# Optimization experiments

Hardware: AMD Instinct MI355X
Metric: run time of the kernel (lower is better)

## Reference

```python
import jax, jax.numpy as jnp
import numpy as np

B, S, D = 4, 2048, 1024
H = 16
DH = D // H

def setup_inputs() -> dict:
    key = jax.random.key(0)
    ks = jax.random.split(key, 5)
    s = 1.0 / np.sqrt(D)
    return {
        "inputs": jax.random.normal(ks[0], (B, S, D), dtype=jnp.float32),
        "Wq": jax.random.normal(ks[1], (D, D), dtype=jnp.float32) * s,
        "Wk": jax.random.normal(ks[2], (D, D), dtype=jnp.float32) * s,
        "Wv": jax.random.normal(ks[3], (D, D), dtype=jnp.float32) * s,
        "Wo": jax.random.normal(ks[4], (D, D), dtype=jnp.float32) * s,
        "bo": jnp.zeros((D,), dtype=jnp.float32),
    }

def reference(inputs, Wq, Wk, Wv, Wo, bo):
    b, s, _ = inputs.shape
    # nn.Linear: y = x @ W.T (no bias for QKV)
    Q = (inputs @ Wq.T).reshape(b, s, H, DH)
    K = (inputs @ Wk.T).reshape(b, s, H, DH)
    V = (inputs @ Wv.T).reshape(b, s, H, DH)
    scores = jnp.einsum("bqhd,bkhd->bhqk", Q, K)  # [B,H,S,S]
    causal = jnp.triu(jnp.ones((s, s), dtype=bool), k=1)
    scores = jnp.where(causal, -jnp.inf, scores)
    w = jax.nn.softmax(scores / np.sqrt(DH), axis=-1)  # dropout p=0.0 -> identity
    Z = jnp.einsum("bhqk,bkhd->bqhd", w, V).reshape(b, s, D)
    return Z @ Wo.T + bo
```

## Files before the change

### kernel.cpp

```cpp
#include <hip/hip_runtime.h>
#include <hip/hip_bf16.h>


#define Bq 4
#define Sq 2048
#define Dq 1024
#define Hq 16
#define DHq 64

typedef __attribute__((ext_vector_type(8))) short short8;
typedef __attribute__((ext_vector_type(4))) float f32x4;
typedef __attribute__((ext_vector_type(4))) unsigned short ushort4v;
typedef __attribute__((ext_vector_type(2))) unsigned int uint2v;

static __device__ __forceinline__ unsigned short f2bfu(float f) {
    union { __hip_bfloat16 h; unsigned short u; } cv;
    cv.h = __float2bfloat16(f);
    return cv.u;
}
static __device__ __forceinline__ unsigned int cvtpk(float lo, float hi) {
    unsigned int r;
    asm("v_cvt_pk_bf16_f32 %0, %1, %2" : "=v"(r) : "v"(lo), "v"(hi));
    return r;
}

__global__ __launch_bounds__(256) void tobf16(
    const float* __restrict__ X, const float* __restrict__ W0,
    const float* __restrict__ W1, const float* __restrict__ W2,
    const float* __restrict__ W3,
    unsigned short* __restrict__ xb, unsigned short* __restrict__ wb)
{
    const size_t i = ((size_t)blockIdx.x * 256 + threadIdx.x) * 8;
    const size_t NX = (size_t)8388608;
    const float* src; unsigned short* dst; size_t off;
    if (i < NX) { src = X; dst = xb; off = i; }
    else {
        const size_t j = i - NX;
        const int w = (int)(j >> 20);
        off = j & 1048575;
        src = (w == 0) ? W0 : (w == 1) ? W1 : (w == 2) ? W2 : W3;
        dst = wb + ((size_t)w << 20);
    }
    const float4 a = *reinterpret_cast<const float4*>(src + off);
    const float4 b = *reinterpret_cast<const float4*>(src + off + 4);
    short8 v;
    v[0] = (short)f2bfu(a.x); v[1] = (short)f2bfu(a.y);
    v[2] = (short)f2bfu(a.z); v[3] = (short)f2bfu(a.w);
    v[4] = (short)f2bfu(b.x); v[5] = (short)f2bfu(b.y);
    v[6] = (short)f2bfu(b.z); v[7] = (short)f2bfu(b.w);
    *reinterpret_cast<short8*>(dst + off) = v;
}



__global__ __launch_bounds__(256) void mm_qkv(
    const unsigned short* __restrict__ Ab, const unsigned short* __restrict__ Wall,
    unsigned short* __restrict__ oq, unsigned short* __restrict__ ok,
    unsigned short* __restrict__ ovt)
{
    __shared__ unsigned short As[128 * 64];
    __shared__ unsigned short Bs[128 * 64];

    const int z = blockIdx.z;
    const unsigned short* W = Wall + ((size_t)z << 20);

    const int m0 = blockIdx.x * 128, n0 = blockIdx.y * 128;
    const int t = threadIdx.x, lane = t & 63, wave = t >> 6;
    const int g = lane >> 4, c = lane & 15;
    const int wm = wave >> 1, wn = wave & 1;
    const int r8 = lane >> 3, c8 = lane & 7;
    const int ss = (c8 ^ (r8 & 7)) * 8;

    f32x4 acc[4][4] = {};

    for (int kt = 0; kt < 16; ++kt) {
        const int kb = kt * 64;
#pragma unroll
        for (int p = 0; p < 4; ++p) {
            const int rowb = wave * 8 + p * 32;
            const unsigned short* ga = Ab + (size_t)(m0 + rowb + r8) * 1024 + kb + ss;
            const unsigned short* gb = W  + (size_t)(n0 + rowb + r8) * 1024 + kb + ss;
            __builtin_amdgcn_global_load_lds(
                (const __attribute__((address_space(1))) unsigned int*)ga,
                (__attribute__((address_space(3))) unsigned int*)(As + rowb * 64), 16, 0, 0);
            __builtin_amdgcn_global_load_lds(
                (const __attribute__((address_space(1))) unsigned int*)gb,
                (__attribute__((address_space(3))) unsigned int*)(Bs + rowb * 64), 16, 0, 0);
        }
        __syncthreads();
        if (z != 2) {
#pragma unroll
            for (int ks = 0; ks < 2; ++ks) {
                const int sa = ((ks * 4 + g) ^ (c & 7)) * 8;
                short8 bf[4];
#pragma unroll
                for (int nt = 0; nt < 4; ++nt)
                    bf[nt] = *reinterpret_cast<const short8*>(&Bs[(wn * 64 + nt * 16 + c) * 64 + sa]);
#pragma unroll
                for (int mt = 0; mt < 4; ++mt) {
                    const short8 af = *reinterpret_cast<const short8*>(&As[(wm * 64 + mt * 16 + c) * 64 + sa]);
#pragma unroll
                    for (int nt = 0; nt < 4; ++nt)
                        acc[mt][nt] = __builtin_amdgcn_mfma_f32_16x16x32_bf16(af, bf[nt], acc[mt][nt], 0, 0, 0);
                }
            }
        } else {
#pragma unroll
            for (int ks = 0; ks < 2; ++ks) {
                const int sa = ((ks * 4 + g) ^ (c & 7)) * 8;
                short8 bf[4];
#pragma unroll
                for (int nt = 0; nt < 4; ++nt)
                    bf[nt] = *reinterpret_cast<const short8*>(&Bs[(wn * 64 + nt * 16 + c) * 64 + sa]);
#pragma unroll
                for (int mt = 0; mt < 4; ++mt) {
                    const short8 af = *reinterpret_cast<const short8*>(&As[(wm * 64 + mt * 16 + c) * 64 + sa]);
#pragma unroll
                    for (int nt = 0; nt < 4; ++nt)
                        acc[mt][nt] = __builtin_amdgcn_mfma_f32_16x16x32_bf16(bf[nt], af, acc[mt][nt], 0, 0, 0);
                }
            }
        }
        __syncthreads();
    }

    if (z == 2) {
#pragma unroll
        for (int mt = 0; mt < 4; ++mt)
#pragma unroll
            for (int nt = 0; nt < 4; ++nt)
#pragma unroll
                for (int r = 0; r < 4; ++r) {
                    const int m = m0 + wm * 64 + mt * 16 + c;
                    const int n = n0 + wn * 64 + nt * 16 + g * 4 + r;
                    const int bb = m >> 11, s = m & 2047;
                    const int h = n >> 6, d = n & 63;
                    const size_t off = (size_t)(bb * Hq + h) * 131072
                        + (s >> 6) * 4096 + ((d >> 4) & 3) * 1024 + ((s >> 5) & 1) * 512
                        + ((s >> 3) & 3) * 128 + (d & 15) * 8 + (s & 7);
                    ovt[off] = f2bfu(acc[mt][nt][r]);
                }
    } else {
        const float oscale = (z == 0) ? 0.180336880f : 1.0f;
        unsigned short* out = z ? ok : oq;
#pragma unroll
        for (int mt = 0; mt < 4; ++mt)
#pragma unroll
            for (int nt = 0; nt < 4; ++nt)
#pragma unroll
                for (int r = 0; r < 4; ++r) {
                    const int m = m0 + wm * 64 + mt * 16 + g * 4 + r;
                    const int n = n0 + wn * 64 + nt * 16 + c;
                    const int bb = m >> 11, s = m & 2047;
                    const int h = n >> 6, d = n & 63;
                    const size_t off = (size_t)(bb * Hq + h) * 131072
                        + (s >> 4) * 1024 + (d >> 5) * 512 + ((d >> 3) & 3) * 128
                        + (s & 15) * 8 + (d & 7);
                    out[off] = f2bfu(acc[mt][nt][r] * oscale);
                }
    }
}

static __device__ __forceinline__ void stage_kv8(
    const unsigned short* __restrict__ Kb, const unsigned short* __restrict__ Vb,
    int kb, unsigned short* kl, unsigned short* vl, int wave, int lane)
{
    const int off = wave * 512 + lane * 8;
    __builtin_amdgcn_global_load_lds(
        (const __attribute__((address_space(1))) unsigned int*)(Kb + (size_t)kb * 4096 + off),
        (__attribute__((address_space(3))) unsigned int*)(kl + wave * 512), 16, 0, 0);
    __builtin_amdgcn_global_load_lds(
        (const __attribute__((address_space(1))) unsigned int*)(Vb + (size_t)kb * 4096 + off),
        (__attribute__((address_space(3))) unsigned int*)(vl + wave * 512), 16, 0, 0);
}

static __device__ __forceinline__ void qtile(
    const short8* kf, const short8* vf, const short8 q0, const short8 q1,
    int rel, int g, int c, unsigned short (*PtW)[72],
    f32x4* oacc, f32x4& lacc, const short8 onesf)
{
    f32x4 st[4] = {};
#pragma unroll
    for (int k2 = 0; k2 < 4; ++k2) {
        st[k2] = __builtin_amdgcn_mfma_f32_16x16x32_bf16(kf[2 * k2],     q0, st[k2], 0, 0, 0);
        st[k2] = __builtin_amdgcn_mfma_f32_16x16x32_bf16(kf[2 * k2 + 1], q1, st[k2], 0, 0, 0);
    }

    if (rel < 4) {
        const int lim = rel * 16 + c;
#pragma unroll
        for (int kt = 0; kt < 4; ++kt)
#pragma unroll
            for (int r = 0; r < 4; ++r)
                if (kt * 16 + g * 4 + r > lim) st[kt][r] = -3.0e38f;
    }

#pragma unroll
    for (int kt = 0; kt < 4; ++kt) {
        uint2v u;
        u[0] = cvtpk(exp2f(st[kt][0]), exp2f(st[kt][1]));
        u[1] = cvtpk(exp2f(st[kt][2]), exp2f(st[kt][3]));
        *reinterpret_cast<uint2v*>(&PtW[c][kt * 16 + g * 4]) = u;
    }
    const short8 pb0 = *reinterpret_cast<const short8*>(&PtW[c][g * 8]);
    const short8 pb1 = *reinterpret_cast<const short8*>(&PtW[c][32 + g * 8]);

#pragma unroll
    for (int dt = 0; dt < 4; ++dt) {
        oacc[dt] = __builtin_amdgcn_mfma_f32_16x16x32_bf16(vf[2 * dt],     pb0, oacc[dt], 0, 0, 0);
        oacc[dt] = __builtin_amdgcn_mfma_f32_16x16x32_bf16(vf[2 * dt + 1], pb1, oacc[dt], 0, 0, 0);
    }
    lacc = __builtin_amdgcn_mfma_f32_16x16x32_bf16(onesf, pb0, lacc, 0, 0, 0);
    lacc = __builtin_amdgcn_mfma_f32_16x16x32_bf16(onesf, pb1, lacc, 0, 0, 0);
}

__global__ __launch_bounds__(512) void attn(
    const unsigned short* __restrict__ Qf, const unsigned short* __restrict__ Kf,
    const unsigned short* __restrict__ Vf, unsigned short* __restrict__ O)
{
    __shared__ unsigned short Kl[2][4096];
    __shared__ unsigned short Vl[2][4096];
    __shared__ unsigned short Pt[8][2][16][72];

    const int bid = blockIdx.x;
    const int pair = (bid >> 3) & 3;
    const int bh = (bid & 7) | ((bid >> 5) << 3);

    const int t = threadIdx.x, lane = t & 63, wave = t >> 6;
    const int g = lane >> 4, c = lane & 15;
    const size_t base = (size_t)bh * (Sq * DHq);
    const unsigned short* Qb = Qf + base;
    const unsigned short* Kb = Kf + base;
    const unsigned short* Vb = Vf + base;
    const int b = bh >> 4, h = bh & 15;

    short8 onesf;
#pragma unroll
    for (int j = 0; j < 8; ++j) onesf[j] = (short)0x3F80;

#pragma unroll 1
    for (int pp = 0; pp < 2; ++pp) {
        const int qi = pp ? (3 - pair) + 4 : pair;
        const int qi2 = pp ? (7 - pair) : pair;
        const int qq = qi2;
        const int qtA = qq * 16 + wave * 2;
        const int qtB = qtA + 1;
        (void)qi;

        const unsigned short* qpA = Qb + (size_t)qtA * 1024 + lane * 8;
        const unsigned short* qpB = Qb + (size_t)qtB * 1024 + lane * 8;
        const short8 qA0 = *reinterpret_cast<const short8*>(qpA);
        const short8 qA1 = *reinterpret_cast<const short8*>(qpA + 512);
        const short8 qB0 = *reinterpret_cast<const short8*>(qpB);
        const short8 qB1 = *reinterpret_cast<const short8*>(qpB + 512);

        f32x4 oA[4] = {}, oB[4] = {};
        f32x4 lA = {}, lB = {};

        const int ibmax = 4 * qq + 3;

        stage_kv8(Kb, Vb, 0, Kl[0], Vl[0], wave, lane);
        __syncthreads();

#pragma unroll 1
        for (int ib = 0; ib <= ibmax; ++ib) {
            const int cur = ib & 1;
            if (ib < ibmax)
                stage_kv8(Kb, Vb, ib + 1, Kl[cur ^ 1], Vl[cur ^ 1], wave, lane);
            __builtin_amdgcn_sched_barrier(0);

            if (4 * ib <= qtB) {
                short8 kf[8], vf[8];
#pragma unroll
                for (int i = 0; i < 8; ++i)
                    kf[i] = *reinterpret_cast<const short8*>(&Kl[cur][lane * 8 + i * 512]);
#pragma unroll
                for (int i = 0; i < 8; ++i)
                    vf[i] = *reinterpret_cast<const short8*>(&Vl[cur][lane * 8 + i * 512]);

                if (4 * ib <= qtA)
                    qtile(kf, vf, qA0, qA1, qtA - 4 * ib, g, c, Pt[wave][0], oA, lA, onesf);
                qtile(kf, vf, qB0, qB1, qtB - 4 * ib, g, c, Pt[wave][1], oB, lB, onesf);
            }
            __syncthreads();
        }

        const float rlA = 1.0f / lA[0];
        const float rlB = 1.0f / lB[0];
        const size_t orowA = ((size_t)b * Sq + qtA * 16 + c) * Dq + h * 64;
        const size_t orowB = ((size_t)b * Sq + qtB * 16 + c) * Dq + h * 64;
#pragma unroll
        for (int dt = 0; dt < 4; ++dt) {
            uint2v uA, uB;
            uA[0] = cvtpk(oA[dt][0] * rlA, oA[dt][1] * rlA);
            uA[1] = cvtpk(oA[dt][2] * rlA, oA[dt][3] * rlA);
            uB[0] = cvtpk(oB[dt][0] * rlB, oB[dt][1] * rlB);
            uB[1] = cvtpk(oB[dt][2] * rlB, oB[dt][3] * rlB);
            *reinterpret_cast<uint2v*>(&O[orowA + dt * 16 + g * 4]) = uA;
            *reinterpret_cast<uint2v*>(&O[orowB + dt * 16 + g * 4]) = uB;
        }
    }
}

__global__ __launch_bounds__(256) void mm_o(
    const unsigned short* __restrict__ Ab, const unsigned short* __restrict__ Wall,
    const float* __restrict__ bo, float* __restrict__ outf)
{
    __shared__ unsigned short As[128 * 64];
    __shared__ unsigned short Bs[128 * 64];

    const unsigned short* W = Wall + ((size_t)3 << 20);

    const int m0 = blockIdx.x * 128, n0 = blockIdx.y * 128;
    const int t = threadIdx.x, lane = t & 63, wave = t >> 6;
    const int g = lane >> 4, c = lane & 15;
    const int wm = wave >> 1, wn = wave & 1;
    const int r8 = lane >> 3, c8 = lane & 7;
    const int ss = (c8 ^ (r8 & 7)) * 8;

    f32x4 acc[4][4] = {};

    for (int kt = 0; kt < 16; ++kt) {
        const int kb = kt * 64;
#pragma unroll
        for (int p = 0; p < 4; ++p) {
            const int rowb = wave * 8 + p * 32;
            const unsigned short* ga = Ab + (size_t)(m0 + rowb + r8) * 1024 + kb + ss;
            const unsigned short* gb = W  + (size_t)(n0 + rowb + r8) * 1024 + kb + ss;
            __builtin_amdgcn_global_load_lds(
                (const __attribute__((address_space(1))) unsigned int*)ga,
                (__attribute__((address_space(3))) unsigned int*)(As + rowb * 64), 16, 0, 0);
            __builtin_amdgcn_global_load_lds(
                (const __attribute__((address_space(1))) unsigned int*)gb,
                (__attribute__((address_space(3))) unsigned int*)(Bs + rowb * 64), 16, 0, 0);
        }
        __syncthreads();
#pragma unroll
        for (int ks = 0; ks < 2; ++ks) {
            const int sa = ((ks * 4 + g) ^ (c & 7)) * 8;
            short8 bf[4];
#pragma unroll
            for (int nt = 0; nt < 4; ++nt)
                bf[nt] = *reinterpret_cast<const short8*>(&Bs[(wn * 64 + nt * 16 + c) * 64 + sa]);
#pragma unroll
            for (int mt = 0; mt < 4; ++mt) {
                const short8 af = *reinterpret_cast<const short8*>(&As[(wm * 64 + mt * 16 + c) * 64 + sa]);
#pragma unroll
                for (int nt = 0; nt < 4; ++nt)
                    acc[mt][nt] = __builtin_amdgcn_mfma_f32_16x16x32_bf16(af, bf[nt], acc[mt][nt], 0, 0, 0);
            }
        }
        __syncthreads();
    }

#pragma unroll
    for (int nt = 0; nt < 4; ++nt) {
        const int n = n0 + wn * 64 + nt * 16 + c;
        const float bias = bo[n];
#pragma unroll
        for (int mt = 0; mt < 4; ++mt)
#pragma unroll
            for (int r = 0; r < 4; ++r) {
                const int m = m0 + wm * 64 + mt * 16 + g * 4 + r;
                outf[(size_t)m * 1024 + n] = acc[mt][nt][r] + bias;
            }
    }
}

extern "C" void kernel_launch(void* const* d_in, const int* in_sizes, int n_in,
                              void* d_out, int out_size, void* d_ws, size_t ws_size,
                              hipStream_t stream) {
    const float* X  = (const float*)d_in[0];
    const float* Wq = (const float*)d_in[1];
    const float* Wk = (const float*)d_in[2];
    const float* Wv = (const float*)d_in[3];
    const float* Wo = (const float*)d_in[4];
    const float* bo = (const float*)d_in[5];
    float* out = (float*)d_out;

    const size_t elems = (size_t)Bq * Hq * Sq * DHq;
    unsigned short* q  = (unsigned short*)d_ws;
    unsigned short* k  = q + elems;
    unsigned short* vt = k + elems;
    unsigned short* xo = vt + elems;
    unsigned short* wb = xo + elems;

    tobf16<<<dim3(6144), 256, 0, stream>>>(X, Wq, Wk, Wv, Wo, xo, wb);

    mm_qkv<<<dim3(64, 8, 3), 256, 0, stream>>>(xo, wb, q, k, vt);

    attn<<<dim3(256), 512, 0, stream>>>(q, k, vt, xo);

    mm_o<<<dim3(64, 8, 1), 256, 0, stream>>>(xo, wb, bo, out);
}
```

Baseline: 187.5 us.

## Split attention blocks to one query chunk each and load V fragments lazily

The attention kernel no longer processes a balanced pair of query chunks per block. It launches 512 blocks with one 256-row query chunk each, ordered heaviest-first. V fragments are now read from LDS inside qtile just before their MFMAs rather than preloaded into registers, and launch bounds request 4 waves per SIMD to raise occupancy. This trades the pairwise causal load balancing for more parallelism and lower register pressure, but blocks now have uneven work and V may be re-read from LDS for each of the two q-tiles.

```diff
diff --git a/kernel.cpp b/kernel.cpp
--- a/kernel.cpp
+++ b/kernel.cpp
@@ -175,8 +175,9 @@
 }
 
 static __device__ __forceinline__ void qtile(
-    const short8* kf, const short8* vf, const short8 q0, const short8 q1,
-    int rel, int g, int c, unsigned short (*PtW)[72],
+    const short8* kf, const unsigned short* __restrict__ vl,
+    const short8 q0, const short8 q1,
+    int rel, int g, int c, int lane, unsigned short (*PtW)[72],
     f32x4* oacc, f32x4& lacc, const short8 onesf)
 {
     f32x4 st[4] = {};
@@ -207,14 +208,16 @@
 
 #pragma unroll
     for (int dt = 0; dt < 4; ++dt) {
-        oacc[dt] = __builtin_amdgcn_mfma_f32_16x16x32_bf16(vf[2 * dt],     pb0, oacc[dt], 0, 0, 0);
-        oacc[dt] = __builtin_amdgcn_mfma_f32_16x16x32_bf16(vf[2 * dt + 1], pb1, oacc[dt], 0, 0, 0);
+        const short8 vf0 = *reinterpret_cast<const short8*>(&vl[lane * 8 + (2 * dt) * 512]);
+        const short8 vf1 = *reinterpret_cast<const short8*>(&vl[lane * 8 + (2 * dt + 1) * 512]);
+        oacc[dt] = __builtin_amdgcn_mfma_f32_16x16x32_bf16(vf0, pb0, oacc[dt], 0, 0, 0);
+        oacc[dt] = __builtin_amdgcn_mfma_f32_16x16x32_bf16(vf1, pb1, oacc[dt], 0, 0, 0);
     }
     lacc = __builtin_amdgcn_mfma_f32_16x16x32_bf16(onesf, pb0, lacc, 0, 0, 0);
     lacc = __builtin_amdgcn_mfma_f32_16x16x32_bf16(onesf, pb1, lacc, 0, 0, 0);
 }
 
-__global__ __launch_bounds__(512) void attn(
+__global__ __launch_bounds__(512, 4) void attn(
     const unsigned short* __restrict__ Qf, const unsigned short* __restrict__ Kf,
     const unsigned short* __restrict__ Vf, unsigned short* __restrict__ O)
 {
@@ -223,8 +226,8 @@
     __shared__ unsigned short Pt[8][2][16][72];
 
     const int bid = blockIdx.x;
-    const int pair = (bid >> 3) & 3;
-    const int bh = (bid & 7) | ((bid >> 5) << 3);
+    const int qq = 7 - ((bid >> 3) & 7);
+    const int bh = (bid & 7) | ((bid >> 6) << 3);
 
     const int t = threadIdx.x, lane = t & 63, wave = t >> 6;
     const int g = lane >> 4, c = lane & 15;
@@ -238,67 +241,57 @@
 #pragma unroll
     for (int j = 0; j < 8; ++j) onesf[j] = (short)0x3F80;
 
+    const int qtA = qq * 16 + wave * 2;
+    const int qtB = qtA + 1;
+
+    const unsigned short* qpA = Qb + (size_t)qtA * 1024 + lane * 8;
+    const unsigned short* qpB = Qb + (size_t)qtB * 1024 + lane * 8;
+    const short8 qA0 = *reinterpret_cast<const short8*>(qpA);
+    const short8 qA1 = *reinterpret_cast<const short8*>(qpA + 512);
+    const short8 qB0 = *reinterpret_cast<const short8*>(qpB);
+    const short8 qB1 = *reinterpret_cast<const short8*>(qpB + 512);
+
+    f32x4 oA[4] = {}, oB[4] = {};
+    f32x4 lA = {}, lB = {};
+
+    const int ibmax = 4 * qq + 3;
+
+    stage_kv8(Kb, Vb, 0, Kl[0], Vl[0], wave, lane);
+    __syncthreads();
+
 #pragma unroll 1
-    for (int pp = 0; pp < 2; ++pp) {
-        const int qi = pp ? (3 - pair) + 4 : pair;
-        const int qi2 = pp ? (7 - pair) : pair;
-        const int qq = qi2;
-        const int qtA = qq * 16 + wave * 2;
-        const int qtB = qtA + 1;
-        (void)qi;
-
-        const unsigned short* qpA = Qb + (size_t)qtA * 1024 + lane * 8;
-        const unsigned short* qpB = Qb + (size_t)qtB * 1024 + lane * 8;
-        const short8 qA0 = *reinterpret_cast<const short8*>(qpA);
-        const short8 qA1 = *reinterpret_cast<const short8*>(qpA + 512);
-        const short8 qB0 = *reinterpret_cast<const short8*>(qpB);
-        const short8 qB1 = *reinterpret_cast<const short8*>(qpB + 512);
-
-        f32x4 oA[4] = {}, oB[4] = {};
-        f32x4 lA = {}, lB = {};
-
-        const int ibmax = 4 * qq + 3;
-
-        stage_kv8(Kb, Vb, 0, Kl[0], Vl[0], wave, lane);
-        __syncthreads();
-
-#pragma unroll 1
-        for (int ib = 0; ib <= ibmax; ++ib) {
-            const int cur = ib & 1;
-            if (ib < ibmax)
-                stage_kv8(Kb, Vb, ib + 1, Kl[cur ^ 1], Vl[cur ^ 1], wave, lane);
-            __builtin_amdgcn_sched_barrier(0);
-
-            if (4 * ib <= qtB) {
-                short8 kf[8], vf[8];
-#pragma unroll
-                for (int i = 0; i < 8; ++i)
-                    kf[i] = *reinterpret_cast<const short8*>(&Kl[cur][lane * 8 + i * 512]);
-#pragma unroll
-                for (int i = 0; i < 8; ++i)
-                    vf[i] = *reinterpret_cast<const short8*>(&Vl[cur][lane * 8 + i * 512]);
-
-                if (4 * ib <= qtA)
-                    qtile(kf, vf, qA0, qA1, qtA - 4 * ib, g, c, Pt[wave][0], oA, lA, onesf);
-                qtile(kf, vf, qB0, qB1, qtB - 4 * ib, g, c, Pt[wave][1], oB, lB, onesf);
-            }
-            __syncthreads();
-        }
-
-        const float rlA = 1.0f / lA[0];
-        const float rlB = 1.0f / lB[0];
-        const size_t orowA = ((size_t)b * Sq + qtA * 16 + c) * Dq + h * 64;
-        const size_t orowB = ((size_t)b * Sq + qtB * 16 + c) * Dq + h * 64;
-#pragma unroll
-        for (int dt = 0; dt < 4; ++dt) {
-            uint2v uA, uB;
-            uA[0] = cvtpk(oA[dt][0] * rlA, oA[dt][1] * rlA);
-            uA[1] = cvtpk(oA[dt][2] * rlA, oA[dt][3] * rlA);
-            uB[0] = cvtpk(oB[dt][0] * rlB, oB[dt][1] * rlB);
-            uB[1] = cvtpk(oB[dt][2] * rlB, oB[dt][3] * rlB);
-            *reinterpret_cast<uint2v*>(&O[orowA + dt * 16 + g * 4]) = uA;
-            *reinterpret_cast<uint2v*>(&O[orowB + dt * 16 + g * 4]) = uB;
-        }
+    for (int ib = 0; ib <= ibmax; ++ib) {
+        const int cur = ib & 1;
+        if (ib < ibmax)
+            stage_kv8(Kb, Vb, ib + 1, Kl[cur ^ 1], Vl[cur ^ 1], wave, lane);
+        __builtin_amdgcn_sched_barrier(0);
+
+        if (4 * ib <= qtB) {
+            short8 kf[8];
+#pragma unroll
+            for (int i = 0; i < 8; ++i)
+                kf[i] = *reinterpret_cast<const short8*>(&Kl[cur][lane * 8 + i * 512]);
+
+            if (4 * ib <= qtA)
+                qtile(kf, Vl[cur], qA0, qA1, qtA - 4 * ib, g, c, lane, Pt[wave][0], oA, lA, onesf);
+            qtile(kf, Vl[cur], qB0, qB1, qtB - 4 * ib, g, c, lane, Pt[wave][1], oB, lB, onesf);
+        }
+        __syncthreads();
+    }
+
+    const float rlA = 1.0f / lA[0];
+    const float rlB = 1.0f / lB[0];
+    const size_t orowA = ((size_t)b * Sq + qtA * 16 + c) * Dq + h * 64;
+    const size_t orowB = ((size_t)b * Sq + qtB * 16 + c) * Dq + h * 64;
+#pragma unroll
+    for (int dt = 0; dt < 4; ++dt) {
+        uint2v uA, uB;
+        uA[0] = cvtpk(oA[dt][0] * rlA, oA[dt][1] * rlA);
+        uA[1] = cvtpk(oA[dt][2] * rlA, oA[dt][3] * rlA);
+        uB[0] = cvtpk(oB[dt][0] * rlB, oB[dt][1] * rlB);
+        uB[1] = cvtpk(oB[dt][2] * rlB, oB[dt][3] * rlB);
+        *reinterpret_cast<uint2v*>(&O[orowA + dt * 16 + g * 4]) = uA;
+        *reinterpret_cast<uint2v*>(&O[orowB + dt * 16 + g * 4]) = uB;
     }
 }
 
@@ -389,7 +382,7 @@
 
     mm_qkv<<<dim3(64, 8, 3), 256, 0, stream>>>(xo, wb, q, k, vt);
 
-    attn<<<dim3(256), 512, 0, stream>>>(q, k, vt, xo);
+    attn<<<dim3(512), 512, 0, stream>>>(q, k, vt, xo);
 
     mm_o<<<dim3(64, 8, 1), 256, 0, stream>>>(xo, wb, bo, out);
 }
```

Result: slower. 208.7 us (+11.3%).
